# Kernel optimization log

Measured on AMD Instinct MI355X. Metric: run time of the kernel, lower is better.

## Reference

```python
import jax, jax.numpy as jnp
import numpy as np

EPS = 1e-06

def feature_map(x):
    # elu(x) + 1, strictly positive
    return jax.nn.elu(x) + 1.0

def setup_inputs() -> dict:
    key = jax.random.key(0)
    k1, k2, k3 = jax.random.split(key, 3)
    n, s, h, d = 8, 8192, 8, 64
    return {
        "queries": jax.random.normal(k1, (n, s, h, d), dtype=jnp.float32),
        "keys": jax.random.normal(k2, (n, s, h, d), dtype=jnp.float32),
        "values": jax.random.normal(k3, (n, s, h, d), dtype=jnp.float32),
        "h": 128,
        "w": 64,
    }

def reference(queries, keys, values, h, w):
    Q = feature_map(queries)            # [n, l, h, d]
    K = feature_map(keys)               # [n, s, h, d]
    # KV outer-product summed over sequence: [n, h, m, d]
    KV = jnp.einsum('nshd,nshm->nhmd', K, values)
    # normalizer: Q . sum_s K   -> [n, l, h]
    Z = 1.0 / (jnp.einsum('nlhd,nhd->nlh', Q, K.sum(axis=1)) + EPS)
    # output: [n, l, h, m]
    V = jnp.einsum('nlhd,nhmd,nlh->nlhm', Q, KV, Z)
    return V
```

## Files before the change

kernel.cpp:

```cpp
#include <hip/hip_runtime.h>
#include <math.h>


#define N_B 8
#define S_LEN 8192
#define H_N 8
#define D_DIM 64
#define NH (N_B * H_N)
#define EPS 1e-6f
#define ROWSTRIDE (H_N * D_DIM)
#define NCHUNK 32
#define CROWS (S_LEN / NCHUNK)
#define TS 64
#define TILES (CROWS / TS)

typedef __attribute__((ext_vector_type(8)))  __bf16 bf16x8;
typedef __attribute__((ext_vector_type(4)))  float  f32x4;
typedef __attribute__((ext_vector_type(4)))  int    i32x4;

__device__ __forceinline__ float felu1(float x) {
    return x > 0.0f ? x + 1.0f : __expf(x);
}
__device__ __forceinline__ unsigned bfb(float f) {
    __bf16 h = (__bf16)f;
    return (unsigned)__builtin_bit_cast(unsigned short, h);
}
__device__ __forceinline__ int pack2bf(float a, float b) {
    return (int)(bfb(a) | (bfb(b) << 16));
}

__global__ __launch_bounds__(256) void kv_partial_kernel(
        const float* __restrict__ Kin, const float* __restrict__ Vin,
        float* __restrict__ kvp,
        float* __restrict__ ksp) {
    __shared__ __align__(16) unsigned int KT[2][64 * 32];
    __shared__ __align__(16) unsigned int VT[2][64 * 32];

    const int b    = blockIdx.x;
    const int h_i  = b & 7;
    const int rest = b >> 3;
    const int c    = rest & (NCHUNK - 1);
    const int n_i  = rest >> 5;
    const int nh   = n_i * H_N + h_i;
    const int ob   = nh * NCHUNK + c;
    const int s0   = c * CROWS;

    const int t = threadIdx.x;
    const int w = t >> 6;
    const int l = t & 63;
    const int d = l;

    const float* Kb = Kin + (size_t)n_i * S_LEN * ROWSTRIDE + (size_t)h_i * D_DIM;
    const float* Vb = Vin + (size_t)n_i * S_LEN * ROWSTRIDE + (size_t)h_i * D_DIM;

    float kraw[16], vraw[16];
    float ksum = 0.0f;

    auto issue = [&](int tile) {
        const size_t base = (size_t)(s0 + tile * TS + w * 8) * ROWSTRIDE + d;
        #pragma unroll
        for (int e = 0; e < 8; ++e) {
            kraw[e] = Kb[base + (size_t)e * ROWSTRIDE];
            vraw[e] = Vb[base + (size_t)e * ROWSTRIDE];
        }
        #pragma unroll
        for (int e = 0; e < 8; ++e) {
            kraw[8 + e] = Kb[base + (size_t)(32 + e) * ROWSTRIDE];
            vraw[8 + e] = Vb[base + (size_t)(32 + e) * ROWSTRIDE];
        }
    };

    auto convwrite = [&](int buf) {
        int kp[8], vp[8];
        #pragma unroll
        for (int p = 0; p < 4; ++p) {
            const float a0 = felu1(kraw[2 * p]);
            const float a1 = felu1(kraw[2 * p + 1]);
            const float b0 = felu1(kraw[8 + 2 * p]);
            const float b1 = felu1(kraw[8 + 2 * p + 1]);
            ksum += (a0 + a1) + (b0 + b1);
            kp[p]     = pack2bf(a0, a1);
            kp[4 + p] = pack2bf(b0, b1);
            vp[p]     = pack2bf(vraw[2 * p],     vraw[2 * p + 1]);
            vp[4 + p] = pack2bf(vraw[8 + 2 * p], vraw[8 + 2 * p + 1]);
        }
        const int gA = ((w)     ^ (d & 7)) * 4;
        const int gB = ((w + 4) ^ (d & 7)) * 4;
        unsigned int* kr = &KT[buf][d * 32];
        unsigned int* vr = &VT[buf][d * 32];
        *(i32x4*)&kr[gA] = (i32x4){kp[0], kp[1], kp[2], kp[3]};
        *(i32x4*)&kr[gB] = (i32x4){kp[4], kp[5], kp[6], kp[7]};
        *(i32x4*)&vr[gA] = (i32x4){vp[0], vp[1], vp[2], vp[3]};
        *(i32x4*)&vr[gB] = (i32x4){vp[4], vp[5], vp[6], vp[7]};
    };

    f32x4 acc[4];
    #pragma unroll
    for (int i = 0; i < 4; ++i) acc[i] = (f32x4){0.f, 0.f, 0.f, 0.f};

    const int arow = 16 * w + (l & 15);
    const int g0   = (((l >> 4))     ^ (l & 7)) * 4;
    const int g1   = ((4 + (l >> 4)) ^ (l & 7)) * 4;
    const int brow = (l & 15);

    auto compute = [&](int buf) {
        const bf16x8 A0 = __builtin_bit_cast(bf16x8, *(const i32x4*)&KT[buf][arow * 32 + g0]);
        const bf16x8 A1 = __builtin_bit_cast(bf16x8, *(const i32x4*)&KT[buf][arow * 32 + g1]);
        #pragma unroll
        for (int mt = 0; mt < 4; ++mt) {
            const int br = (16 * mt + brow) * 32;
            const bf16x8 B0 = __builtin_bit_cast(bf16x8, *(const i32x4*)&VT[buf][br + g0]);
            const bf16x8 B1 = __builtin_bit_cast(bf16x8, *(const i32x4*)&VT[buf][br + g1]);
            acc[mt] = __builtin_amdgcn_mfma_f32_16x16x32_bf16(A0, B0, acc[mt], 0, 0, 0);
            acc[mt] = __builtin_amdgcn_mfma_f32_16x16x32_bf16(A1, B1, acc[mt], 0, 0, 0);
        }
    };

    issue(0);
    convwrite(0);
    issue(1);
    __syncthreads();

    for (int tile = 0; tile < TILES; ++tile) {
        const int cur = tile & 1;
        compute(cur);
        if (tile + 1 < TILES) convwrite(cur ^ 1);
        if (tile + 2 < TILES) issue(tile + 2);
        __syncthreads();
    }

    float* kvo = kvp + (size_t)ob * (D_DIM * D_DIM);
    #pragma unroll
    for (int mt = 0; mt < 4; ++mt) {
        #pragma unroll
        for (int r = 0; r < 4; ++r) {
            const int row = 16 * w + (l >> 4) * 4 + r;
            const int col = 16 * mt + (l & 15);
            kvo[row * 64 + col] = acc[mt][r];
        }
    }

    float* ksl = (float*)&KT[0][0];
    ksl[w * 64 + d] = ksum;
    __syncthreads();
    if (t < D_DIM) {
        ksp[(size_t)ob * D_DIM + t] =
            ksl[t] + ksl[64 + t] + ksl[128 + t] + ksl[192 + t];
    }
}

__global__ __launch_bounds__(256) void kv_reduce_kernel(
        const float* __restrict__ kvp, const float* __restrict__ ksp,
        float* __restrict__ KV, float* __restrict__ Ksum) {
    const int nh = blockIdx.x >> 4;
    const int eb = blockIdx.x & 15;
    const int t  = threadIdx.x;
    const int e  = eb * 256 + t;
    float s = 0.0f;
    const float* base = kvp + (size_t)nh * NCHUNK * (D_DIM * D_DIM) + e;
    #pragma unroll 8
    for (int c = 0; c < NCHUNK; ++c)
        s += base[(size_t)c * (D_DIM * D_DIM)];
    KV[(size_t)nh * (D_DIM * D_DIM) + e] = s;
    if (eb == 0 && t < D_DIM) {
        float ks = 0.0f;
        #pragma unroll 8
        for (int c = 0; c < NCHUNK; ++c)
            ks += ksp[(size_t)nh * NCHUNK * D_DIM + (size_t)c * D_DIM + t];
        Ksum[(size_t)nh * D_DIM + t] = ks;
    }
}

__global__ __launch_bounds__(256) void out_kernel(
        const float* __restrict__ Qin, const float* __restrict__ KV,
        const float* __restrict__ Ksum, float* __restrict__ Out) {
    constexpr int RPB  = 128;
    constexpr int QPAD = 68;
    __shared__ __align__(16) float KVs[D_DIM][D_DIM];
    __shared__ __align__(16) float Kss[D_DIM];
    __shared__ __align__(16) float Qs[RPB][QPAD];

    const int b    = blockIdx.x;
    const int nblk = S_LEN / RPB;
    const int h_i  = b & 7;
    const int rest = b >> 3;
    const int rb   = rest & (nblk - 1);
    const int n_i  = rest >> 6;
    const int nh   = n_i * H_N + h_i;
    const int t    = threadIdx.x;

    const float* Qb = Qin + (size_t)n_i * S_LEN * ROWSTRIDE + (size_t)h_i * D_DIM;
    float*       Ob = Out + (size_t)n_i * S_LEN * ROWSTRIDE + (size_t)h_i * D_DIM;

    {
        const float4* src = (const float4*)(KV + (size_t)nh * (D_DIM * D_DIM));
        float4* dst = (float4*)(&KVs[0][0]);
        #pragma unroll
        for (int i = 0; i < 4; ++i) dst[t + 256 * i] = src[t + 256 * i];
        if (t < 16) ((float4*)Kss)[t] = ((const float4*)(Ksum + (size_t)nh * D_DIM))[t];
    }

    const int ltx = t & 15, lty = t >> 4;
    const int sbase = rb * RPB;
    #pragma unroll
    for (int i = 0; i < 8; ++i) {
        const int row = lty + 16 * i;
        const float4 q = *(const float4*)(Qb + (size_t)(sbase + row) * ROWSTRIDE + ltx * 4);
        float4 f;
        f.x = felu1(q.x); f.y = felu1(q.y); f.z = felu1(q.z); f.w = felu1(q.w);
        const int pc = (ltx * 4) ^ (((row >> 2) & 7) << 2);
        *(float4*)&Qs[row][pc] = f;
    }
    __syncthreads();

    const int rg = t >> 3;
    const int mg = t & 7;
    const int r0 = rg * 4, m0 = mg * 8;
    const int sw = ((rg & 7) << 2);

    float acc[4][8];
    float zz[4];
    #pragma unroll
    for (int r = 0; r < 4; ++r) {
        zz[r] = 0.0f;
        #pragma unroll
        for (int m = 0; m < 8; ++m) acc[r][m] = 0.0f;
    }

    #pragma unroll
    for (int d0 = 0; d0 < D_DIM; d0 += 4) {
        const float4 ks4 = *(const float4*)&Kss[d0];
        float4 qr[4];
        #pragma unroll
        for (int r = 0; r < 4; ++r) {
            qr[r] = *(const float4*)&Qs[r0 + r][d0 ^ sw];
            zz[r] += qr[r].x * ks4.x + qr[r].y * ks4.y
                   + qr[r].z * ks4.z + qr[r].w * ks4.w;
        }
        #pragma unroll
        for (int j = 0; j < 4; ++j) {
            const float4 kva = *(const float4*)&KVs[d0 + j][m0];
            const float4 kvb = *(const float4*)&KVs[d0 + j][m0 + 4];
            #pragma unroll
            for (int r = 0; r < 4; ++r) {
                const float q = (&qr[r].x)[j];
                acc[r][0] += q * kva.x; acc[r][1] += q * kva.y;
                acc[r][2] += q * kva.z; acc[r][3] += q * kva.w;
                acc[r][4] += q * kvb.x; acc[r][5] += q * kvb.y;
                acc[r][6] += q * kvb.z; acc[r][7] += q * kvb.w;
            }
        }
    }

    #pragma unroll
    for (int r = 0; r < 4; ++r) {
        const float z = 1.0f / (zz[r] + EPS);
        float4 o1, o2;
        o1.x = acc[r][0] * z; o1.y = acc[r][1] * z;
        o1.z = acc[r][2] * z; o1.w = acc[r][3] * z;
        o2.x = acc[r][4] * z; o2.y = acc[r][5] * z;
        o2.z = acc[r][6] * z; o2.w = acc[r][7] * z;
        float* op = Ob + (size_t)(sbase + r0 + r) * ROWSTRIDE + m0;
        *(float4*)op       = o1;
        *(float4*)(op + 4) = o2;
    }
}

extern "C" void kernel_launch(void* const* d_in, const int* in_sizes, int n_in,
                              void* d_out, int out_size, void* d_ws, size_t ws_size,
                              hipStream_t stream) {
    const float* q = (const float*)d_in[0];
    const float* k = (const float*)d_in[1];
    const float* v = (const float*)d_in[2];
    float* out = (float*)d_out;

    float* kvp  = (float*)d_ws;
    float* ksp  = kvp + (size_t)NH * NCHUNK * D_DIM * D_DIM;
    float* KVf  = ksp + (size_t)NH * NCHUNK * D_DIM;
    float* Ksum = KVf + (size_t)NH * D_DIM * D_DIM;

    kv_partial_kernel<<<N_B * NCHUNK * H_N, 256, 0, stream>>>(k, v, kvp, ksp);
    kv_reduce_kernel<<<NH * 16, 256, 0, stream>>>(kvp, ksp, KVf, Ksum);
    out_kernel<<<NH * (S_LEN / 128), 256, 0, stream>>>(q, KVf, Ksum, out);
}
```

Baseline: 170.4 us.

## Load K/V rows as float4 and transpose via ds_read_tr with MFMA key sums

Each thread now loads 16 contiguous floats of one sequence row with float4 loads, replacing the strided scalar per-column loads. The tiles are stored row-major in LDS, and the MFMA operands are read with the transposing ds_read_b64_tr_b16 instruction. The per-column key sum is computed by an extra MFMA against a ones vector, replacing the scalar adds and the LDS reduction. The change adds inline asm, explicit waitcnt and barriers, and bf16 rounding of the K sum, which the old code kept in fp32.

```diff
diff --git a/kernel.cpp b/kernel.cpp
--- a/kernel.cpp
+++ b/kernel.cpp
@@ -11,12 +11,13 @@
 #define ROWSTRIDE (H_N * D_DIM)
 #define NCHUNK 32
 #define CROWS (S_LEN / NCHUNK)
-#define TS 64
-#define TILES (CROWS / TS)
+#define RROWS 64
+#define ROUNDS (CROWS / RROWS)
 
 typedef __attribute__((ext_vector_type(8)))  __bf16 bf16x8;
 typedef __attribute__((ext_vector_type(4)))  float  f32x4;
 typedef __attribute__((ext_vector_type(4)))  int    i32x4;
+typedef __attribute__((ext_vector_type(2)))  int    i32x2;
 
 __device__ __forceinline__ float felu1(float x) {
     return x > 0.0f ? x + 1.0f : __expf(x);
@@ -33,100 +34,123 @@
         const float* __restrict__ Kin, const float* __restrict__ Vin,
         float* __restrict__ kvp,
         float* __restrict__ ksp) {
-    __shared__ __align__(16) unsigned int KT[2][64 * 32];
-    __shared__ __align__(16) unsigned int VT[2][64 * 32];
+    __shared__ __align__(16) __bf16 KT[2][4096];
+    __shared__ __align__(16) __bf16 VT[2][4096];
 
     const int b    = blockIdx.x;
     const int h_i  = b & 7;
     const int rest = b >> 3;
     const int c    = rest & (NCHUNK - 1);
     const int n_i  = rest >> 5;
-    const int nh   = n_i * H_N + h_i;
-    const int ob   = nh * NCHUNK + c;
+    const int ob   = (n_i * H_N + h_i) * NCHUNK + c;
     const int s0   = c * CROWS;
 
     const int t = threadIdx.x;
     const int w = t >> 6;
     const int l = t & 63;
-    const int d = l;
 
     const float* Kb = Kin + (size_t)n_i * S_LEN * ROWSTRIDE + (size_t)h_i * D_DIM;
     const float* Vb = Vin + (size_t)n_i * S_LEN * ROWSTRIDE + (size_t)h_i * D_DIM;
 
-    float kraw[16], vraw[16];
-    float ksum = 0.0f;
-
-    auto issue = [&](int tile) {
-        const size_t base = (size_t)(s0 + tile * TS + w * 8) * ROWSTRIDE + d;
-        #pragma unroll
-        for (int e = 0; e < 8; ++e) {
-            kraw[e] = Kb[base + (size_t)e * ROWSTRIDE];
-            vraw[e] = Vb[base + (size_t)e * ROWSTRIDE];
-        }
-        #pragma unroll
-        for (int e = 0; e < 8; ++e) {
-            kraw[8 + e] = Kb[base + (size_t)(32 + e) * ROWSTRIDE];
-            vraw[8 + e] = Vb[base + (size_t)(32 + e) * ROWSTRIDE];
-        }
+    const int srow = t & 63;
+    const int dq   = t >> 6;
+
+    float4 kr[4], vr[4];
+
+    auto issue = [&](int round) {
+        const float* kp = Kb + (size_t)(s0 + round * RROWS + srow) * ROWSTRIDE + dq * 16;
+        const float* vp = Vb + (size_t)(s0 + round * RROWS + srow) * ROWSTRIDE + dq * 16;
+        #pragma unroll
+        for (int i = 0; i < 4; ++i) kr[i] = ((const float4*)kp)[i];
+        #pragma unroll
+        for (int i = 0; i < 4; ++i) vr[i] = ((const float4*)vp)[i];
     };
 
+    const int wbyte = dq * 2048 + (srow >> 2) * 128
+                    + (((srow & 3) ^ ((srow >> 2) & 3)) * 32);
+
     auto convwrite = [&](int buf) {
-        int kp[8], vp[8];
-        #pragma unroll
-        for (int p = 0; p < 4; ++p) {
-            const float a0 = felu1(kraw[2 * p]);
-            const float a1 = felu1(kraw[2 * p + 1]);
-            const float b0 = felu1(kraw[8 + 2 * p]);
-            const float b1 = felu1(kraw[8 + 2 * p + 1]);
-            ksum += (a0 + a1) + (b0 + b1);
-            kp[p]     = pack2bf(a0, a1);
-            kp[4 + p] = pack2bf(b0, b1);
-            vp[p]     = pack2bf(vraw[2 * p],     vraw[2 * p + 1]);
-            vp[4 + p] = pack2bf(vraw[8 + 2 * p], vraw[8 + 2 * p + 1]);
-        }
-        const int gA = ((w)     ^ (d & 7)) * 4;
-        const int gB = ((w + 4) ^ (d & 7)) * 4;
-        unsigned int* kr = &KT[buf][d * 32];
-        unsigned int* vr = &VT[buf][d * 32];
-        *(i32x4*)&kr[gA] = (i32x4){kp[0], kp[1], kp[2], kp[3]};
-        *(i32x4*)&kr[gB] = (i32x4){kp[4], kp[5], kp[6], kp[7]};
-        *(i32x4*)&vr[gA] = (i32x4){vp[0], vp[1], vp[2], vp[3]};
-        *(i32x4*)&vr[gB] = (i32x4){vp[4], vp[5], vp[6], vp[7]};
+        int kp8[8], vp8[8];
+        #pragma unroll
+        for (int i = 0; i < 4; ++i) {
+            kp8[2 * i]     = pack2bf(felu1(kr[i].x), felu1(kr[i].y));
+            kp8[2 * i + 1] = pack2bf(felu1(kr[i].z), felu1(kr[i].w));
+            vp8[2 * i]     = pack2bf(vr[i].x, vr[i].y);
+            vp8[2 * i + 1] = pack2bf(vr[i].z, vr[i].w);
+        }
+        char* kb = (char*)&KT[buf][0] + wbyte;
+        char* vb = (char*)&VT[buf][0] + wbyte;
+        *(i32x4*)kb        = (i32x4){kp8[0], kp8[1], kp8[2], kp8[3]};
+        *(i32x4*)(kb + 16) = (i32x4){kp8[4], kp8[5], kp8[6], kp8[7]};
+        *(i32x4*)vb        = (i32x4){vp8[0], vp8[1], vp8[2], vp8[3]};
+        *(i32x4*)(vb + 16) = (i32x4){vp8[4], vp8[5], vp8[6], vp8[7]};
     };
 
     f32x4 acc[4];
+    f32x4 ksacc = (f32x4){0.f, 0.f, 0.f, 0.f};
     #pragma unroll
     for (int i = 0; i < 4; ++i) acc[i] = (f32x4){0.f, 0.f, 0.f, 0.f};
-
-    const int arow = 16 * w + (l & 15);
-    const int g0   = (((l >> 4))     ^ (l & 7)) * 4;
-    const int g1   = ((4 + (l >> 4)) ^ (l & 7)) * 4;
-    const int brow = (l & 15);
+    const bf16x8 ONES = __builtin_bit_cast(bf16x8,
+        (i32x4){0x3F803F80, 0x3F803F80, 0x3F803F80, 0x3F803F80});
+
+    const int rdlane = (l & 15) * 8 + (l >> 4) * 256;
 
     auto compute = [&](int buf) {
-        const bf16x8 A0 = __builtin_bit_cast(bf16x8, *(const i32x4*)&KT[buf][arow * 32 + g0]);
-        const bf16x8 A1 = __builtin_bit_cast(bf16x8, *(const i32x4*)&KT[buf][arow * 32 + g1]);
+        unsigned kbase, vbase;
+        {
+            auto k3 = (__attribute__((address_space(3))) char*)&KT[buf][0];
+            auto v3 = (__attribute__((address_space(3))) char*)&VT[buf][0];
+            kbase = (unsigned)(size_t)k3 + rdlane;
+            vbase = (unsigned)(size_t)v3 + rdlane;
+        }
+        bf16x8 A[2];
+        {
+            const unsigned ka = kbase + w * 2048;
+            i32x2 r0, r1, r2, r3;
+            asm volatile("ds_read_b64_tr_b16 %0, %4\n\t"
+                         "ds_read_b64_tr_b16 %1, %4 offset:128\n\t"
+                         "ds_read_b64_tr_b16 %2, %4 offset:1024\n\t"
+                         "ds_read_b64_tr_b16 %3, %4 offset:1152"
+                         : "=&v"(r0), "=&v"(r1), "=&v"(r2), "=&v"(r3) : "v"(ka));
+            asm volatile("s_waitcnt lgkmcnt(0)" ::: "memory");
+            __builtin_amdgcn_sched_barrier(0);
+            A[0] = __builtin_bit_cast(bf16x8, (i32x4){r0.x, r0.y, r1.x, r1.y});
+            A[1] = __builtin_bit_cast(bf16x8, (i32x4){r2.x, r2.y, r3.x, r3.y});
+        }
+        ksacc = __builtin_amdgcn_mfma_f32_16x16x32_bf16(A[0], ONES, ksacc, 0, 0, 0);
+        ksacc = __builtin_amdgcn_mfma_f32_16x16x32_bf16(A[1], ONES, ksacc, 0, 0, 0);
         #pragma unroll
         for (int mt = 0; mt < 4; ++mt) {
-            const int br = (16 * mt + brow) * 32;
-            const bf16x8 B0 = __builtin_bit_cast(bf16x8, *(const i32x4*)&VT[buf][br + g0]);
-            const bf16x8 B1 = __builtin_bit_cast(bf16x8, *(const i32x4*)&VT[buf][br + g1]);
-            acc[mt] = __builtin_amdgcn_mfma_f32_16x16x32_bf16(A0, B0, acc[mt], 0, 0, 0);
-            acc[mt] = __builtin_amdgcn_mfma_f32_16x16x32_bf16(A1, B1, acc[mt], 0, 0, 0);
+            const unsigned va = vbase + mt * 2048;
+            i32x2 b0, b1, b2, b3;
+            asm volatile("ds_read_b64_tr_b16 %0, %4\n\t"
+                         "ds_read_b64_tr_b16 %1, %4 offset:128\n\t"
+                         "ds_read_b64_tr_b16 %2, %4 offset:1024\n\t"
+                         "ds_read_b64_tr_b16 %3, %4 offset:1152"
+                         : "=&v"(b0), "=&v"(b1), "=&v"(b2), "=&v"(b3) : "v"(va));
+            asm volatile("s_waitcnt lgkmcnt(0)" ::: "memory");
+            __builtin_amdgcn_sched_barrier(0);
+            const bf16x8 B0 = __builtin_bit_cast(bf16x8, (i32x4){b0.x, b0.y, b1.x, b1.y});
+            const bf16x8 B1 = __builtin_bit_cast(bf16x8, (i32x4){b2.x, b2.y, b3.x, b3.y});
+            acc[mt] = __builtin_amdgcn_mfma_f32_16x16x32_bf16(A[0], B0, acc[mt], 0, 0, 0);
+            acc[mt] = __builtin_amdgcn_mfma_f32_16x16x32_bf16(A[1], B1, acc[mt], 0, 0, 0);
         }
     };
 
     issue(0);
     convwrite(0);
     issue(1);
-    __syncthreads();
-
-    for (int tile = 0; tile < TILES; ++tile) {
-        const int cur = tile & 1;
-        compute(cur);
-        if (tile + 1 < TILES) convwrite(cur ^ 1);
-        if (tile + 2 < TILES) issue(tile + 2);
-        __syncthreads();
+    asm volatile("s_waitcnt lgkmcnt(0)" ::: "memory");
+    __builtin_amdgcn_s_barrier();
+
+    for (int r = 0; r < ROUNDS; ++r) {
+        compute(r & 1);
+        if (r + 1 < ROUNDS) {
+            convwrite((r + 1) & 1);
+            if (r + 2 < ROUNDS) issue(r + 2);
+        }
+        asm volatile("s_waitcnt lgkmcnt(0)" ::: "memory");
+        __builtin_amdgcn_s_barrier();
     }
 
     float* kvo = kvp + (size_t)ob * (D_DIM * D_DIM);
@@ -139,13 +163,10 @@
             kvo[row * 64 + col] = acc[mt][r];
         }
     }
-
-    float* ksl = (float*)&KT[0][0];
-    ksl[w * 64 + d] = ksum;
-    __syncthreads();
-    if (t < D_DIM) {
-        ksp[(size_t)ob * D_DIM + t] =
-            ksl[t] + ksl[64 + t] + ksl[128 + t] + ksl[192 + t];
+    if ((l & 15) == 0) {
+        #pragma unroll
+        for (int r = 0; r < 4; ++r)
+            ksp[(size_t)ob * D_DIM + 16 * w + (l >> 4) * 4 + r] = ksacc[r];
     }
 }
 
```

New measurement: 185.5 us. 8.9% more time.

## Restructure KV partial kernel into 128-row rounds with 64 chunks when workspace allows

Applied to the files above, without the earlier changes.

The KV partial kernel now has each thread load 32 rows of K and V in one batch and processes 128-row rounds with a single LDS buffer, replacing the 64-row double-buffered tile pipeline. When the workspace is large enough it splits the sequence into 64 chunks of 128 rows, doubling the grid to raise parallelism and memory-level parallelism. A fallback keeps 32 chunks with two rounds each. The cost is more partial KV data to write and reduce, more registers per thread, and no overlap between loads and MFMA within a block.

```diff
diff --git a/kernel.cpp b/kernel.cpp
--- a/kernel.cpp
+++ b/kernel.cpp
@@ -9,10 +9,6 @@
 #define NH (N_B * H_N)
 #define EPS 1e-6f
 #define ROWSTRIDE (H_N * D_DIM)
-#define NCHUNK 32
-#define CROWS (S_LEN / NCHUNK)
-#define TS 64
-#define TILES (CROWS / TS)
 
 typedef __attribute__((ext_vector_type(8)))  __bf16 bf16x8;
 typedef __attribute__((ext_vector_type(4)))  float  f32x4;
@@ -29,69 +25,60 @@
     return (int)(bfb(a) | (bfb(b) << 16));
 }
 
+template<int ROUNDS>
 __global__ __launch_bounds__(256) void kv_partial_kernel(
         const float* __restrict__ Kin, const float* __restrict__ Vin,
         float* __restrict__ kvp,
         float* __restrict__ ksp) {
-    __shared__ __align__(16) unsigned int KT[2][64 * 32];
-    __shared__ __align__(16) unsigned int VT[2][64 * 32];
+    constexpr int NCH  = 64 / ROUNDS;
+    constexpr int CLOG = (ROUNDS == 1) ? 6 : 5;
+    __shared__ __align__(16) unsigned KT[64 * 64];
+    __shared__ __align__(16) unsigned VT[64 * 64];
 
     const int b    = blockIdx.x;
     const int h_i  = b & 7;
     const int rest = b >> 3;
-    const int c    = rest & (NCHUNK - 1);
-    const int n_i  = rest >> 5;
-    const int nh   = n_i * H_N + h_i;
-    const int ob   = nh * NCHUNK + c;
-    const int s0   = c * CROWS;
+    const int c    = rest & (NCH - 1);
+    const int n_i  = rest >> CLOG;
+    const int ob   = (n_i * H_N + h_i) * NCH + c;
+    const int s0   = c * (ROUNDS * 128);
 
     const int t = threadIdx.x;
     const int w = t >> 6;
     const int l = t & 63;
-    const int d = l;
 
     const float* Kb = Kin + (size_t)n_i * S_LEN * ROWSTRIDE + (size_t)h_i * D_DIM;
     const float* Vb = Vin + (size_t)n_i * S_LEN * ROWSTRIDE + (size_t)h_i * D_DIM;
 
-    float kraw[16], vraw[16];
+    float kraw[32], vraw[32];
     float ksum = 0.0f;
 
-    auto issue = [&](int tile) {
-        const size_t base = (size_t)(s0 + tile * TS + w * 8) * ROWSTRIDE + d;
-        #pragma unroll
-        for (int e = 0; e < 8; ++e) {
-            kraw[e] = Kb[base + (size_t)e * ROWSTRIDE];
-            vraw[e] = Vb[base + (size_t)e * ROWSTRIDE];
-        }
-        #pragma unroll
-        for (int e = 0; e < 8; ++e) {
-            kraw[8 + e] = Kb[base + (size_t)(32 + e) * ROWSTRIDE];
-            vraw[8 + e] = Vb[base + (size_t)(32 + e) * ROWSTRIDE];
-        }
+    auto issue = [&](int r) {
+        const size_t base = (size_t)(s0 + r * 128 + 32 * w) * ROWSTRIDE + l;
+        #pragma unroll
+        for (int e = 0; e < 32; ++e) kraw[e] = Kb[base + (size_t)e * ROWSTRIDE];
+        #pragma unroll
+        for (int e = 0; e < 32; ++e) vraw[e] = Vb[base + (size_t)e * ROWSTRIDE];
     };
 
-    auto convwrite = [&](int buf) {
-        int kp[8], vp[8];
-        #pragma unroll
-        for (int p = 0; p < 4; ++p) {
+    auto convwrite = [&]() {
+        int kp[16], vp[16];
+        #pragma unroll
+        for (int p = 0; p < 16; ++p) {
             const float a0 = felu1(kraw[2 * p]);
             const float a1 = felu1(kraw[2 * p + 1]);
-            const float b0 = felu1(kraw[8 + 2 * p]);
-            const float b1 = felu1(kraw[8 + 2 * p + 1]);
-            ksum += (a0 + a1) + (b0 + b1);
-            kp[p]     = pack2bf(a0, a1);
-            kp[4 + p] = pack2bf(b0, b1);
-            vp[p]     = pack2bf(vraw[2 * p],     vraw[2 * p + 1]);
-            vp[4 + p] = pack2bf(vraw[8 + 2 * p], vraw[8 + 2 * p + 1]);
-        }
-        const int gA = ((w)     ^ (d & 7)) * 4;
-        const int gB = ((w + 4) ^ (d & 7)) * 4;
-        unsigned int* kr = &KT[buf][d * 32];
-        unsigned int* vr = &VT[buf][d * 32];
-        *(i32x4*)&kr[gA] = (i32x4){kp[0], kp[1], kp[2], kp[3]};
-        *(i32x4*)&kr[gB] = (i32x4){kp[4], kp[5], kp[6], kp[7]};
-        *(i32x4*)&vr[gA] = (i32x4){vp[0], vp[1], vp[2], vp[3]};
-        *(i32x4*)&vr[gB] = (i32x4){vp[4], vp[5], vp[6], vp[7]};
+            ksum += a0 + a1;
+            kp[p] = pack2bf(a0, a1);
+            vp[p] = pack2bf(vraw[2 * p], vraw[2 * p + 1]);
+        }
+        unsigned* kr = &KT[l * 64 + (w >> 1) * 32];
+        unsigned* vr = &VT[l * 64 + (w >> 1) * 32];
+        #pragma unroll
+        for (int j = 0; j < 4; ++j) {
+            const int po = ((4 * (w & 1) + j) ^ (l & 7)) * 4;
+            *(i32x4*)&kr[po] = (i32x4){kp[4*j], kp[4*j+1], kp[4*j+2], kp[4*j+3]};
+            *(i32x4*)&vr[po] = (i32x4){vp[4*j], vp[4*j+1], vp[4*j+2], vp[4*j+3]};
+        }
     };
 
     f32x4 acc[4];
@@ -99,34 +86,34 @@
     for (int i = 0; i < 4; ++i) acc[i] = (f32x4){0.f, 0.f, 0.f, 0.f};
 
     const int arow = 16 * w + (l & 15);
-    const int g0   = (((l >> 4))     ^ (l & 7)) * 4;
-    const int g1   = ((4 + (l >> 4)) ^ (l & 7)) * 4;
-    const int brow = (l & 15);
-
-    auto compute = [&](int buf) {
-        const bf16x8 A0 = __builtin_bit_cast(bf16x8, *(const i32x4*)&KT[buf][arow * 32 + g0]);
-        const bf16x8 A1 = __builtin_bit_cast(bf16x8, *(const i32x4*)&KT[buf][arow * 32 + g1]);
-        #pragma unroll
-        for (int mt = 0; mt < 4; ++mt) {
-            const int br = (16 * mt + brow) * 32;
-            const bf16x8 B0 = __builtin_bit_cast(bf16x8, *(const i32x4*)&VT[buf][br + g0]);
-            const bf16x8 B1 = __builtin_bit_cast(bf16x8, *(const i32x4*)&VT[buf][br + g1]);
-            acc[mt] = __builtin_amdgcn_mfma_f32_16x16x32_bf16(A0, B0, acc[mt], 0, 0, 0);
-            acc[mt] = __builtin_amdgcn_mfma_f32_16x16x32_bf16(A1, B1, acc[mt], 0, 0, 0);
+    auto compute = [&]() {
+        #pragma unroll
+        for (int sub = 0; sub < 2; ++sub) {
+            #pragma unroll
+            for (int ks = 0; ks < 2; ++ks) {
+                const int g = ((4 * ks + (l >> 4)) ^ (l & 7)) * 4;
+                const bf16x8 A = __builtin_bit_cast(bf16x8,
+                    *(const i32x4*)&KT[arow * 64 + sub * 32 + g]);
+                #pragma unroll
+                for (int mt = 0; mt < 4; ++mt) {
+                    const bf16x8 B = __builtin_bit_cast(bf16x8,
+                        *(const i32x4*)&VT[(16 * mt + (l & 15)) * 64 + sub * 32 + g]);
+                    acc[mt] = __builtin_amdgcn_mfma_f32_16x16x32_bf16(A, B, acc[mt], 0, 0, 0);
+                }
+            }
         }
     };
 
     issue(0);
-    convwrite(0);
-    issue(1);
-    __syncthreads();
-
-    for (int tile = 0; tile < TILES; ++tile) {
-        const int cur = tile & 1;
-        compute(cur);
-        if (tile + 1 < TILES) convwrite(cur ^ 1);
-        if (tile + 2 < TILES) issue(tile + 2);
+    #pragma unroll
+    for (int r = 0; r < ROUNDS; ++r) {
+        convwrite();
         __syncthreads();
+        compute();
+        if (r + 1 < ROUNDS) {
+            issue(r + 1);
+            __syncthreads();
+        }
     }
 
     float* kvo = kvp + (size_t)ob * (D_DIM * D_DIM);
@@ -140,8 +127,9 @@
         }
     }
 
-    float* ksl = (float*)&KT[0][0];
-    ksl[w * 64 + d] = ksum;
+    __syncthreads();
+    float* ksl = (float*)&KT[0];
+    ksl[w * 64 + l] = ksum;
     __syncthreads();
     if (t < D_DIM) {
         ksp[(size_t)ob * D_DIM + t] =
@@ -149,6 +137,7 @@
     }
 }
 
+template<int NCH>
 __global__ __launch_bounds__(256) void kv_reduce_kernel(
         const float* __restrict__ kvp, const float* __restrict__ ksp,
         float* __restrict__ KV, float* __restrict__ Ksum) {
@@ -157,16 +146,16 @@
     const int t  = threadIdx.x;
     const int e  = eb * 256 + t;
     float s = 0.0f;
-    const float* base = kvp + (size_t)nh * NCHUNK * (D_DIM * D_DIM) + e;
+    const float* base = kvp + (size_t)nh * NCH * (D_DIM * D_DIM) + e;
     #pragma unroll 8
-    for (int c = 0; c < NCHUNK; ++c)
+    for (int c = 0; c < NCH; ++c)
         s += base[(size_t)c * (D_DIM * D_DIM)];
     KV[(size_t)nh * (D_DIM * D_DIM) + e] = s;
     if (eb == 0 && t < D_DIM) {
         float ks = 0.0f;
         #pragma unroll 8
-        for (int c = 0; c < NCHUNK; ++c)
-            ks += ksp[(size_t)nh * NCHUNK * D_DIM + (size_t)c * D_DIM + t];
+        for (int c = 0; c < NCH; ++c)
+            ks += ksp[(size_t)nh * NCH * D_DIM + (size_t)c * D_DIM + t];
         Ksum[(size_t)nh * D_DIM + t] = ks;
     }
 }
@@ -274,12 +263,26 @@
     const float* v = (const float*)d_in[2];
     float* out = (float*)d_out;
 
-    float* kvp  = (float*)d_ws;
-    float* ksp  = kvp + (size_t)NH * NCHUNK * D_DIM * D_DIM;
-    float* KVf  = ksp + (size_t)NH * NCHUNK * D_DIM;
-    float* Ksum = KVf + (size_t)NH * D_DIM * D_DIM;
-
-    kv_partial_kernel<<<N_B * NCHUNK * H_N, 256, 0, stream>>>(k, v, kvp, ksp);
-    kv_reduce_kernel<<<NH * 16, 256, 0, stream>>>(kvp, ksp, KVf, Ksum);
-    out_kernel<<<NH * (S_LEN / 128), 256, 0, stream>>>(q, KVf, Ksum, out);
-}
+    const size_t need64 = ((size_t)NH * 64 * (4096 + 64)
+                         + (size_t)NH * (4096 + 64)) * sizeof(float);
+
+    if (ws_size >= need64) {
+        const int nch = 64;
+        float* kvp  = (float*)d_ws;
+        float* ksp  = kvp + (size_t)NH * nch * D_DIM * D_DIM;
+        float* KVf  = ksp + (size_t)NH * nch * D_DIM;
+        float* Ksum = KVf + (size_t)NH * D_DIM * D_DIM;
+        kv_partial_kernel<1><<<N_B * nch * H_N, 256, 0, stream>>>(k, v, kvp, ksp);
+        kv_reduce_kernel<64><<<NH * 16, 256, 0, stream>>>(kvp, ksp, KVf, Ksum);
+        out_kernel<<<NH * (S_LEN / 128), 256, 0, stream>>>(q, KVf, Ksum, out);
+    } else {
+        const int nch = 32;
+        float* kvp  = (float*)d_ws;
+        float* ksp  = kvp + (size_t)NH * nch * D_DIM * D_DIM;
+        float* KVf  = ksp + (size_t)NH * nch * D_DIM;
+        float* Ksum = KVf + (size_t)NH * D_DIM * D_DIM;
+        kv_partial_kernel<2><<<N_B * nch * H_N, 256, 0, stream>>>(k, v, kvp, ksp);
+        kv_reduce_kernel<32><<<NH * 16, 256, 0, stream>>>(kvp, ksp, KVf, Ksum);
+        out_kernel<<<NH * (S_LEN / 128), 256, 0, stream>>>(q, KVf, Ksum, out);
+    }
+}
```

Result: no change. 169.2 us (-0.7%).
